# Kernel tuning notes

Measured on AMD Instinct MI355X. Metric: run time of the kernel, lower is better.

Reference implementation:

```python
import jax, jax.numpy as jnp
import numpy as np
from jax.scipy.special import logsumexp

N = 4096
TAU = 2.0
IT = 30


def setup_inputs() -> dict:
    key = jax.random.key(0)
    k1, k2 = jax.random.split(key)
    eps = jax.random.normal(k1, (N, N), dtype=jnp.float32)
    mean = jax.random.uniform(k2, (N, N), dtype=jnp.float32)
    std = 10.0 * jnp.ones((N, N), dtype=jnp.float32)  # matches nn.Parameter(10*ones)
    return {"eps": eps, "mean": mean, "std": std}


def reference(eps, mean, std):
    # P_noisy = mean + std * eps ; Sinkhorn-Knopp in log domain, then exp.
    A = (mean + std * eps) / TAU

    def step(A, _):
        A = A - logsumexp(A, axis=1, keepdims=True)  # row normalize (log domain)
        A = A - logsumexp(A, axis=0, keepdims=True)  # col normalize (log domain)
        return A, None

    A, _ = jax.lax.scan(step, A, None, length=IT)
    return jnp.exp(A)
```

## Files before the change

### kernel.cpp

```cpp
#include <hip/hip_runtime.h>


constexpr int N    = 4096;
constexpr int IT   = 30;
constexpr int NBLK = 512;
constexpr int TPB  = 512;

typedef __attribute__((ext_vector_type(8))) unsigned short ushort8v;
typedef __attribute__((ext_vector_type(4))) unsigned short ushort4v;

__device__ inline float bf2f(unsigned int h) {
    union { unsigned int u; float f; } x; x.u = h << 16; return x.f;
}
__device__ inline unsigned short f2bf(float f) {
    union { float f; unsigned int u; } x; x.f = f;
    unsigned int r = x.u + 0x7FFFu + ((x.u >> 16) & 1u);
    return (unsigned short)(r >> 16);
}

struct V8 { float v[8]; };
struct V4 { float v[4]; };

template<typename PT>
__device__ inline V8 loadP8(const PT* base, int e);
template<> __device__ inline V8 loadP8<unsigned short>(const unsigned short* base, int e) {
    ushort8v p = *(const ushort8v*)(base + e);
    V8 r;
    #pragma unroll
    for (int k = 0; k < 8; ++k) r.v[k] = bf2f((unsigned int)p[k]);
    return r;
}
template<> __device__ inline V8 loadP8<float>(const float* base, int e) {
    float4 a = *(const float4*)(base + e);
    float4 b = *(const float4*)(base + e + 4);
    V8 r = {{a.x, a.y, a.z, a.w, b.x, b.y, b.z, b.w}};
    return r;
}

template<typename PT>
__device__ inline V4 loadP4(const PT* base, size_t e);
template<> __device__ inline V4 loadP4<unsigned short>(const unsigned short* base, size_t e) {
    ushort4v p = *(const ushort4v*)(base + e);
    V4 r;
    #pragma unroll
    for (int k = 0; k < 4; ++k) r.v[k] = bf2f((unsigned int)p[k]);
    return r;
}
template<> __device__ inline V4 loadP4<float>(const float* base, size_t e) {
    float4 a = *(const float4*)(base + e);
    V4 r = {{a.x, a.y, a.z, a.w}};
    return r;
}

template<typename PT>
__global__ __launch_bounds__(512) void k_init(const float* __restrict__ eps,
                                              const float* __restrict__ mean,
                                              const float* __restrict__ stdv,
                                              PT* __restrict__ P,
                                              float* __restrict__ bufA) {
    const int idx = blockIdx.x * 512 + threadIdx.x;
    const float4 e = ((const float4*)eps )[(size_t)idx];
    const float4 m = ((const float4*)mean)[(size_t)idx];
    const float4 s = ((const float4*)stdv)[(size_t)idx];
    float p[4];
    p[0] = __expf((m.x + s.x * e.x) * 0.5f);
    p[1] = __expf((m.y + s.y * e.y) * 0.5f);
    p[2] = __expf((m.z + s.z * e.z) * 0.5f);
    p[3] = __expf((m.w + s.w * e.w) * 0.5f);
    if constexpr (sizeof(PT) == 2) {
        ushort4v o;
        #pragma unroll
        for (int k = 0; k < 4; ++k) o[k] = f2bf(p[k]);
        *(ushort4v*)((unsigned short*)P + 4 * (size_t)idx) = o;
    } else {
        float4 a = {p[0], p[1], p[2], p[3]};
        ((float4*)P)[(size_t)idx] = a;
    }
    if (idx < N) bufA[idx] = 1.0f;
}

template<typename PT>
__global__ __launch_bounds__(TPB) void k_iter(const PT* __restrict__ P,
                                              const float* __restrict__ csum_prev,
                                              float* __restrict__ partial,
                                              float* __restrict__ u_glob) {
    __shared__ float ldsRow[8][8];
    __shared__ float ldsU[8];
    const int t    = threadIdx.x;
    const int wv   = t >> 6, lane = t & 63;
    const int b    = blockIdx.x;
    const int col0 = t * 8;
    const int q    = t * 4;
    const int row0 = b * 8;

    float4 c0 = *(const float4*)&csum_prev[q];
    float4 c1 = *(const float4*)&csum_prev[2048 + q];
    float v[8];
    v[0] = __builtin_amdgcn_rcpf(c0.x);  v[1] = __builtin_amdgcn_rcpf(c0.y);
    v[2] = __builtin_amdgcn_rcpf(c0.z);  v[3] = __builtin_amdgcn_rcpf(c0.w);
    v[4] = __builtin_amdgcn_rcpf(c1.x);  v[5] = __builtin_amdgcn_rcpf(c1.y);
    v[6] = __builtin_amdgcn_rcpf(c1.z);  v[7] = __builtin_amdgcn_rcpf(c1.w);

    V8 pf[8];
    #pragma unroll
    for (int i = 0; i < 8; ++i)
        pf[i] = loadP8(P + (size_t)(row0 + i) * N, col0);

    #pragma unroll
    for (int i = 0; i < 8; ++i) {
        float s = pf[i].v[0] * v[0] + pf[i].v[1] * v[1] + pf[i].v[2] * v[2] + pf[i].v[3] * v[3]
                + pf[i].v[4] * v[4] + pf[i].v[5] * v[5] + pf[i].v[6] * v[6] + pf[i].v[7] * v[7];
        #pragma unroll
        for (int off = 32; off; off >>= 1) s += __shfl_xor(s, off, 64);
        if (lane == 0) ldsRow[i][wv] = s;
    }
    __syncthreads();

    if (t < 64) {
        const int row = t >> 3, w = t & 7;
        float s = ldsRow[row][w];
        s += __shfl_xor(s, 1, 64);
        s += __shfl_xor(s, 2, 64);
        s += __shfl_xor(s, 4, 64);
        if (w == 0) {
            float u = __builtin_amdgcn_rcpf(s);
            ldsU[row] = u;
            u_glob[row0 + row] = u;
        }
    }
    __syncthreads();

    float acc[8] = {0, 0, 0, 0, 0, 0, 0, 0};
    #pragma unroll
    for (int i = 0; i < 8; ++i) {
        const float u = ldsU[i];
        #pragma unroll
        for (int k = 0; k < 8; ++k) acc[k] += u * pf[i].v[k];
    }
    float4 a  = {acc[0], acc[1], acc[2], acc[3]};
    float4 bb = {acc[4], acc[5], acc[6], acc[7]};
    *(float4*)&partial[(size_t)b * N + q]        = a;
    *(float4*)&partial[(size_t)b * N + 2048 + q] = bb;
}

__global__ __launch_bounds__(512) void k_reduce(const float* __restrict__ partial,
                                                float* __restrict__ csum_cur) {
    __shared__ float red[8][64];
    const int t = threadIdx.x;
    const int lane = t & 63, wv = t >> 6;
    const int col = blockIdx.x * 64 + lane;
    float s = 0.0f;
    const float* p = partial + (size_t)(wv * 64) * N + col;
    #pragma unroll 8
    for (int b = 0; b < 64; ++b)
        s += p[(size_t)b * N];
    red[wv][lane] = s;
    __syncthreads();
    if (t < 64) {
        float acc = 0.0f;
        #pragma unroll
        for (int w = 0; w < 8; ++w) acc += red[w][t];
        csum_cur[blockIdx.x * 64 + t] = acc;
    }
}

template<typename PT>
__global__ __launch_bounds__(256) void k_final(const PT* __restrict__ P,
                                               const float* __restrict__ u_glob,
                                               const float* __restrict__ csum_last,
                                               float* __restrict__ out) {
    const int idx = blockIdx.x * 256 + threadIdx.x;
    const int row = idx >> 10;
    const int c4  = (idx & 1023) * 4;
    const float u = u_glob[row];
    const int perm = ((c4 & 4) ? 2048 : 0) + ((c4 >> 3) << 2);
    float4 cc = *(const float4*)&csum_last[perm];
    V4 p = loadP4(P, (size_t)row * N + c4);
    float4 r;
    r.x = p.v[0] * u * __builtin_amdgcn_rcpf(cc.x);
    r.y = p.v[1] * u * __builtin_amdgcn_rcpf(cc.y);
    r.z = p.v[2] * u * __builtin_amdgcn_rcpf(cc.z);
    r.w = p.v[3] * u * __builtin_amdgcn_rcpf(cc.w);
    ((float4*)out)[(size_t)idx] = r;
}

extern "C" void kernel_launch(void* const* d_in, const int* in_sizes, int n_in,
                              void* d_out, int out_size, void* d_ws, size_t ws_size,
                              hipStream_t stream) {
    const float* eps  = (const float*)d_in[0];
    const float* mean = (const float*)d_in[1];
    const float* stdv = (const float*)d_in[2];
    float* out = (float*)d_out;
    char* ws = (char*)d_ws;

    float* bufA   = (float*)ws;
    float* bufB   = bufA + N;
    float* u_glob = bufB + N;
    const size_t partOff = 64 * 1024;
    float* partial = (float*)(ws + partOff);
    const size_t partBytes = (size_t)NBLK * N * sizeof(float);
    const size_t pOff   = partOff + partBytes;
    const size_t pBytes = (size_t)N * N * sizeof(unsigned short);

    const int initGrid  = N * N / 4 / 512;
    const int finalGrid = N * N / 4 / 256;

    float* cs[2] = { bufA, bufB };

    if (ws_size >= pOff + pBytes) {
        unsigned short* P = (unsigned short*)(ws + pOff);
        k_init<unsigned short><<<initGrid, 512, 0, stream>>>(eps, mean, stdv, P, bufA);
        for (int t = 1; t <= IT; ++t) {
            k_iter<unsigned short><<<NBLK, TPB, 0, stream>>>(P, cs[(t - 1) & 1], partial, u_glob);
            k_reduce<<<64, 512, 0, stream>>>(partial, cs[t & 1]);
        }
        k_final<unsigned short><<<finalGrid, 256, 0, stream>>>(P, u_glob, cs[IT & 1], out);
    } else {
        float* P = out;
        k_init<float><<<initGrid, 512, 0, stream>>>(eps, mean, stdv, P, bufA);
        for (int t = 1; t <= IT; ++t) {
            k_iter<float><<<NBLK, TPB, 0, stream>>>(P, cs[(t - 1) & 1], partial, u_glob);
            k_reduce<<<64, 512, 0, stream>>>(partial, cs[t & 1]);
        }
        k_final<float><<<finalGrid, 256, 0, stream>>>(P, u_glob, cs[IT & 1], out);
    }
}
```

Before: 642.0 us.

## Fuse init into first Sinkhorn iteration and double rows per block

Replaces the separate init kernel with a k_first kernel. It computes exp((mean+std*eps)/tau), stores P, and does the first row/column normalization from the same registers, which drops one read of P. Rows per block go from 8 to 16 and the grid from 512 to 256 blocks, halving the partial column-sum buffer that k_reduce must read each iteration. k_reduce is reorganized into 128 blocks of 32 columns with 16 slices. Register pressure rises from holding 16 rows per thread, and there are fewer blocks to spread across CUs.

```diff
diff --git a/kernel.cpp b/kernel.cpp
--- a/kernel.cpp
+++ b/kernel.cpp
@@ -3,11 +3,11 @@
 
 constexpr int N    = 4096;
 constexpr int IT   = 30;
-constexpr int NBLK = 512;
+constexpr int NBLK = 256;
+constexpr int ROWS = 16;
 constexpr int TPB  = 512;
 
 typedef __attribute__((ext_vector_type(8))) unsigned short ushort8v;
-typedef __attribute__((ext_vector_type(4))) unsigned short ushort4v;
 
 __device__ inline float bf2f(unsigned int h) {
     union { unsigned int u; float f; } x; x.u = h << 16; return x.f;
@@ -21,22 +21,19 @@
 struct V8 { float v[8]; };
 struct V4 { float v[4]; };
 
-template<typename PT>
-__device__ inline V8 loadP8(const PT* base, int e);
-template<> __device__ inline V8 loadP8<unsigned short>(const unsigned short* base, int e) {
-    ushort8v p = *(const ushort8v*)(base + e);
+template<typename PT> struct StoreOf;
+template<> struct StoreOf<unsigned short> { using T = ushort8v; };
+template<> struct StoreOf<float>          { using T = V8;       };
+
+__device__ inline V8 unpackP(const ushort8v& s) {
     V8 r;
     #pragma unroll
-    for (int k = 0; k < 8; ++k) r.v[k] = bf2f((unsigned int)p[k]);
+    for (int k = 0; k < 8; ++k) r.v[k] = bf2f((unsigned int)s[k]);
     return r;
 }
-template<> __device__ inline V8 loadP8<float>(const float* base, int e) {
-    float4 a = *(const float4*)(base + e);
-    float4 b = *(const float4*)(base + e + 4);
-    V8 r = {{a.x, a.y, a.z, a.w, b.x, b.y, b.z, b.w}};
-    return r;
-}
-
+__device__ inline V8 unpackP(const V8& s) { return s; }
+
+typedef __attribute__((ext_vector_type(4))) unsigned short ushort4v;
 template<typename PT>
 __device__ inline V4 loadP4(const PT* base, size_t e);
 template<> __device__ inline V4 loadP4<unsigned short>(const unsigned short* base, size_t e) {
@@ -53,70 +50,65 @@
 }
 
 template<typename PT>
-__global__ __launch_bounds__(512) void k_init(const float* __restrict__ eps,
-                                              const float* __restrict__ mean,
-                                              const float* __restrict__ stdv,
-                                              PT* __restrict__ P,
-                                              float* __restrict__ bufA) {
-    const int idx = blockIdx.x * 512 + threadIdx.x;
-    const float4 e = ((const float4*)eps )[(size_t)idx];
-    const float4 m = ((const float4*)mean)[(size_t)idx];
-    const float4 s = ((const float4*)stdv)[(size_t)idx];
-    float p[4];
-    p[0] = __expf((m.x + s.x * e.x) * 0.5f);
-    p[1] = __expf((m.y + s.y * e.y) * 0.5f);
-    p[2] = __expf((m.z + s.z * e.z) * 0.5f);
-    p[3] = __expf((m.w + s.w * e.w) * 0.5f);
-    if constexpr (sizeof(PT) == 2) {
-        ushort4v o;
-        #pragma unroll
-        for (int k = 0; k < 4; ++k) o[k] = f2bf(p[k]);
-        *(ushort4v*)((unsigned short*)P + 4 * (size_t)idx) = o;
-    } else {
-        float4 a = {p[0], p[1], p[2], p[3]};
-        ((float4*)P)[(size_t)idx] = a;
-    }
-    if (idx < N) bufA[idx] = 1.0f;
-}
-
-template<typename PT>
-__global__ __launch_bounds__(TPB) void k_iter(const PT* __restrict__ P,
-                                              const float* __restrict__ csum_prev,
-                                              float* __restrict__ partial,
-                                              float* __restrict__ u_glob) {
-    __shared__ float ldsRow[8][8];
-    __shared__ float ldsU[8];
+__global__ __launch_bounds__(TPB) void k_first(const float* __restrict__ eps,
+                                               const float* __restrict__ mean,
+                                               const float* __restrict__ stdv,
+                                               PT* __restrict__ P,
+                                               float* __restrict__ partial,
+                                               float* __restrict__ u_glob) {
+    __shared__ float ldsRow[ROWS][8];
+    __shared__ float ldsU[ROWS];
     const int t    = threadIdx.x;
     const int wv   = t >> 6, lane = t & 63;
     const int b    = blockIdx.x;
     const int col0 = t * 8;
     const int q    = t * 4;
-    const int row0 = b * 8;
-
-    float4 c0 = *(const float4*)&csum_prev[q];
-    float4 c1 = *(const float4*)&csum_prev[2048 + q];
-    float v[8];
-    v[0] = __builtin_amdgcn_rcpf(c0.x);  v[1] = __builtin_amdgcn_rcpf(c0.y);
-    v[2] = __builtin_amdgcn_rcpf(c0.z);  v[3] = __builtin_amdgcn_rcpf(c0.w);
-    v[4] = __builtin_amdgcn_rcpf(c1.x);  v[5] = __builtin_amdgcn_rcpf(c1.y);
-    v[6] = __builtin_amdgcn_rcpf(c1.z);  v[7] = __builtin_amdgcn_rcpf(c1.w);
-
-    V8 pf[8];
-    #pragma unroll
-    for (int i = 0; i < 8; ++i)
-        pf[i] = loadP8(P + (size_t)(row0 + i) * N, col0);
-
-    #pragma unroll
-    for (int i = 0; i < 8; ++i) {
-        float s = pf[i].v[0] * v[0] + pf[i].v[1] * v[1] + pf[i].v[2] * v[2] + pf[i].v[3] * v[3]
-                + pf[i].v[4] * v[4] + pf[i].v[5] * v[5] + pf[i].v[6] * v[6] + pf[i].v[7] * v[7];
+    const int row0 = b * ROWS;
+
+    typename StoreOf<PT>::T raw[ROWS];
+
+    #pragma unroll
+    for (int i = 0; i < ROWS; ++i) {
+        const size_t rb = (size_t)(row0 + i) * N + col0;
+        float4 e0 = *(const float4*)&eps [rb], e1 = *(const float4*)&eps [rb + 4];
+        float4 m0 = *(const float4*)&mean[rb], m1 = *(const float4*)&mean[rb + 4];
+        float4 s0 = *(const float4*)&stdv[rb], s1 = *(const float4*)&stdv[rb + 4];
+        float p[8];
+        p[0] = __expf((m0.x + s0.x * e0.x) * 0.5f);
+        p[1] = __expf((m0.y + s0.y * e0.y) * 0.5f);
+        p[2] = __expf((m0.z + s0.z * e0.z) * 0.5f);
+        p[3] = __expf((m0.w + s0.w * e0.w) * 0.5f);
+        p[4] = __expf((m1.x + s1.x * e1.x) * 0.5f);
+        p[5] = __expf((m1.y + s1.y * e1.y) * 0.5f);
+        p[6] = __expf((m1.z + s1.z * e1.z) * 0.5f);
+        p[7] = __expf((m1.w + s1.w * e1.w) * 0.5f);
+        if constexpr (sizeof(PT) == 2) {
+            ushort8v o;
+            #pragma unroll
+            for (int k = 0; k < 8; ++k) o[k] = f2bf(p[k]);
+            raw[i] = o;
+            *(ushort8v*)((unsigned short*)P + rb) = o;
+        } else {
+            V8 r = {{p[0], p[1], p[2], p[3], p[4], p[5], p[6], p[7]}};
+            raw[i] = r;
+            float4 a = {p[0], p[1], p[2], p[3]}, bb = {p[4], p[5], p[6], p[7]};
+            *(float4*)((float*)P + rb)     = a;
+            *(float4*)((float*)P + rb + 4) = bb;
+        }
+    }
+
+    #pragma unroll
+    for (int i = 0; i < ROWS; ++i) {
+        V8 pf = unpackP(raw[i]);
+        float s = pf.v[0] + pf.v[1] + pf.v[2] + pf.v[3]
+                + pf.v[4] + pf.v[5] + pf.v[6] + pf.v[7];
         #pragma unroll
         for (int off = 32; off; off >>= 1) s += __shfl_xor(s, off, 64);
         if (lane == 0) ldsRow[i][wv] = s;
     }
     __syncthreads();
 
-    if (t < 64) {
+    if (t < 8 * ROWS) {
         const int row = t >> 3, w = t & 7;
         float s = ldsRow[row][w];
         s += __shfl_xor(s, 1, 64);
@@ -132,10 +124,11 @@
 
     float acc[8] = {0, 0, 0, 0, 0, 0, 0, 0};
     #pragma unroll
-    for (int i = 0; i < 8; ++i) {
+    for (int i = 0; i < ROWS; ++i) {
         const float u = ldsU[i];
-        #pragma unroll
-        for (int k = 0; k < 8; ++k) acc[k] += u * pf[i].v[k];
+        V8 pf = unpackP(raw[i]);
+        #pragma unroll
+        for (int k = 0; k < 8; ++k) acc[k] += u * pf.v[k];
     }
     float4 a  = {acc[0], acc[1], acc[2], acc[3]};
     float4 bb = {acc[4], acc[5], acc[6], acc[7]};
@@ -143,24 +136,91 @@
     *(float4*)&partial[(size_t)b * N + 2048 + q] = bb;
 }
 
+template<typename PT>
+__global__ __launch_bounds__(TPB) void k_iter(const PT* __restrict__ P,
+                                              const float* __restrict__ csum_prev,
+                                              float* __restrict__ partial,
+                                              float* __restrict__ u_glob) {
+    __shared__ float ldsRow[ROWS][8];
+    __shared__ float ldsU[ROWS];
+    const int t    = threadIdx.x;
+    const int wv   = t >> 6, lane = t & 63;
+    const int b    = blockIdx.x;
+    const int col0 = t * 8;
+    const int q    = t * 4;
+    const int row0 = b * ROWS;
+
+    float4 c0 = *(const float4*)&csum_prev[q];
+    float4 c1 = *(const float4*)&csum_prev[2048 + q];
+    float v[8];
+    v[0] = __builtin_amdgcn_rcpf(c0.x);  v[1] = __builtin_amdgcn_rcpf(c0.y);
+    v[2] = __builtin_amdgcn_rcpf(c0.z);  v[3] = __builtin_amdgcn_rcpf(c0.w);
+    v[4] = __builtin_amdgcn_rcpf(c1.x);  v[5] = __builtin_amdgcn_rcpf(c1.y);
+    v[6] = __builtin_amdgcn_rcpf(c1.z);  v[7] = __builtin_amdgcn_rcpf(c1.w);
+
+    typename StoreOf<PT>::T raw[ROWS];
+    #pragma unroll
+    for (int i = 0; i < ROWS; ++i)
+        raw[i] = *(const typename StoreOf<PT>::T*)(P + (size_t)(row0 + i) * N + col0);
+
+    #pragma unroll
+    for (int i = 0; i < ROWS; ++i) {
+        V8 pf = unpackP(raw[i]);
+        float s = pf.v[0] * v[0] + pf.v[1] * v[1] + pf.v[2] * v[2] + pf.v[3] * v[3]
+                + pf.v[4] * v[4] + pf.v[5] * v[5] + pf.v[6] * v[6] + pf.v[7] * v[7];
+        #pragma unroll
+        for (int off = 32; off; off >>= 1) s += __shfl_xor(s, off, 64);
+        if (lane == 0) ldsRow[i][wv] = s;
+    }
+    __syncthreads();
+
+    if (t < 8 * ROWS) {
+        const int row = t >> 3, w = t & 7;
+        float s = ldsRow[row][w];
+        s += __shfl_xor(s, 1, 64);
+        s += __shfl_xor(s, 2, 64);
+        s += __shfl_xor(s, 4, 64);
+        if (w == 0) {
+            float u = __builtin_amdgcn_rcpf(s);
+            ldsU[row] = u;
+            u_glob[row0 + row] = u;
+        }
+    }
+    __syncthreads();
+
+    float acc[8] = {0, 0, 0, 0, 0, 0, 0, 0};
+    #pragma unroll
+    for (int i = 0; i < ROWS; ++i) {
+        const float u = ldsU[i];
+        V8 pf = unpackP(raw[i]);
+        #pragma unroll
+        for (int k = 0; k < 8; ++k) acc[k] += u * pf.v[k];
+    }
+    float4 a  = {acc[0], acc[1], acc[2], acc[3]};
+    float4 bb = {acc[4], acc[5], acc[6], acc[7]};
+    *(float4*)&partial[(size_t)b * N + q]        = a;
+    *(float4*)&partial[(size_t)b * N + 2048 + q] = bb;
+}
+
 __global__ __launch_bounds__(512) void k_reduce(const float* __restrict__ partial,
                                                 float* __restrict__ csum_cur) {
-    __shared__ float red[8][64];
+    __shared__ float red[16][32];
     const int t = threadIdx.x;
     const int lane = t & 63, wv = t >> 6;
-    const int col = blockIdx.x * 64 + lane;
+    const int c     = blockIdx.x * 32 + (lane & 31);
+    const int slice = wv * 2 + (lane >> 5);
+    const float* p = partial + (size_t)(slice * 16) * N + c;
     float s = 0.0f;
-    const float* p = partial + (size_t)(wv * 64) * N + col;
-    #pragma unroll 8
-    for (int b = 0; b < 64; ++b)
-        s += p[(size_t)b * N];
-    red[wv][lane] = s;
-    __syncthreads();
-    if (t < 64) {
+    #pragma unroll 16
+    for (int r = 0; r < 16; ++r)
+        s += p[(size_t)r * N];
+    red[slice][lane & 31] = s;
+    __syncthreads();
+    if (t < 32) {
         float acc = 0.0f;
         #pragma unroll
-        for (int w = 0; w < 8; ++w) acc += red[w][t];
-        csum_cur[blockIdx.x * 64 + t] = acc;
+        for (int sl = 0; sl < 16; ++sl) acc += red[sl][t];
+        csum_cur[blockIdx.x * 32 + t] = acc;
     }
 }
 
@@ -202,25 +262,26 @@
     const size_t pOff   = partOff + partBytes;
     const size_t pBytes = (size_t)N * N * sizeof(unsigned short);
 
-    const int initGrid  = N * N / 4 / 512;
     const int finalGrid = N * N / 4 / 256;
 
     float* cs[2] = { bufA, bufB };
 
     if (ws_size >= pOff + pBytes) {
         unsigned short* P = (unsigned short*)(ws + pOff);
-        k_init<unsigned short><<<initGrid, 512, 0, stream>>>(eps, mean, stdv, P, bufA);
-        for (int t = 1; t <= IT; ++t) {
+        k_first<unsigned short><<<NBLK, TPB, 0, stream>>>(eps, mean, stdv, P, partial, u_glob);
+        k_reduce<<<128, 512, 0, stream>>>(partial, cs[1]);
+        for (int t = 2; t <= IT; ++t) {
             k_iter<unsigned short><<<NBLK, TPB, 0, stream>>>(P, cs[(t - 1) & 1], partial, u_glob);
-            k_reduce<<<64, 512, 0, stream>>>(partial, cs[t & 1]);
+            k_reduce<<<128, 512, 0, stream>>>(partial, cs[t & 1]);
         }
         k_final<unsigned short><<<finalGrid, 256, 0, stream>>>(P, u_glob, cs[IT & 1], out);
     } else {
         float* P = out;
-        k_init<float><<<initGrid, 512, 0, stream>>>(eps, mean, stdv, P, bufA);
-        for (int t = 1; t <= IT; ++t) {
+        k_first<float><<<NBLK, TPB, 0, stream>>>(eps, mean, stdv, P, partial, u_glob);
+        k_reduce<<<128, 512, 0, stream>>>(partial, cs[1]);
+        for (int t = 2; t <= IT; ++t) {
             k_iter<float><<<NBLK, TPB, 0, stream>>>(P, cs[(t - 1) & 1], partial, u_glob);
-            k_reduce<<<64, 512, 0, stream>>>(partial, cs[t & 1]);
+            k_reduce<<<128, 512, 0, stream>>>(partial, cs[t & 1]);
         }
         k_final<float><<<finalGrid, 256, 0, stream>>>(P, u_glob, cs[IT & 1], out);
     }
```

Result: faster. 586.2 us (-8.7%).
